# Kernel optimization log

Measured on AMD Instinct MI355X. Metric: run time of the kernel, lower is better.

Reference implementation:

```python
import jax, jax.numpy as jnp
import numpy as np

S, B, IN, H, NLAYERS = 2048, 1024, 4, 4, 6  # 3 stacked nn.LSTM modules x num_layers=2 each


def setup_inputs() -> dict:
    key = jax.random.key(0)
    ks = jax.random.split(key, 7)
    scale = 1.0 / np.sqrt(H)  # PyTorch LSTM init range
    return {
        "x": jax.random.normal(ks[0], (S, B, IN), jnp.float32),
        "w_ih": jax.random.uniform(ks[1], (NLAYERS, 4 * H, H), jnp.float32, -scale, scale),
        "w_hh": jax.random.uniform(ks[2], (NLAYERS, 4 * H, H), jnp.float32, -scale, scale),
        "b_ih": jax.random.uniform(ks[3], (NLAYERS, 4 * H), jnp.float32, -scale, scale),
        "b_hh": jax.random.uniform(ks[4], (NLAYERS, 4 * H), jnp.float32, -scale, scale),
        "reg_w": jax.random.uniform(ks[5], (1, H), jnp.float32, -scale, scale),
        "reg_b": jax.random.uniform(ks[6], (1,), jnp.float32, -scale, scale),
    }


def _lstm_layer(x, w_ih, w_hh, b_ih, b_hh):
    # x: [S, B, H_in]; PyTorch gate order: input, forget, cell(g), output
    b = x.shape[1]
    pre = jnp.einsum('sbi,gi->sbg', x, w_ih) + b_ih + b_hh  # [S, B, 4H], input projection hoisted out of scan

    def step(carry, p):
        h, c = carry
        gates = p + h @ w_hh.T
        i, f, g, o = jnp.split(gates, 4, axis=-1)
        c = jax.nn.sigmoid(f) * c + jax.nn.sigmoid(i) * jnp.tanh(g)
        h = jax.nn.sigmoid(o) * jnpat(c) if False else jax.nn.sigmoid(o) * jnp.tanh(c)
        return (h, c), h

    h0 = jnp.zeros((b, H), x.dtype)
    (_, _), ys = jax.lax.scan(step, (h0, h0), pre)
    return ys  # [S, B, H]


def reference(x, w_ih, w_hh, b_ih, b_hh, reg_w, reg_b):
    # 6 stacked LSTM layers (lstm1: layers 0-1, lstm2: 2-3, lstm3: 4-5).
    # Dropout (p=0.02) between layers and dropout3 are identity in eval mode.
    y = x
    for l in range(NLAYERS):
        y = _lstm_layer(y, w_ih[l], w_hh[l], b_ih[l], b_hh[l])
    out = jnp.einsum('sbh,oh->sbo', y, reg_w) + reg_b  # linear head, [S, B, 1]
    return out
```

## Files before the change

kernel.cpp:

```cpp
#include <hip/hip_runtime.h>

#define S_LEN  2048
#define BATCH  1024
#define NL     6
#define CH     16

typedef float f32x2 __attribute__((ext_vector_type(2)));

__device__ __forceinline__ float fexp2(float x) { return __builtin_amdgcn_exp2f(x); }
__device__ __forceinline__ float frcp(float x)  { return __builtin_amdgcn_rcpf(x); }

template <int CTRL>
__device__ __forceinline__ float dppf(float v) {
    return __int_as_float(__builtin_amdgcn_update_dpp(
        0, __float_as_int(v), CTRL, 0xF, 0xF, true));
}
__device__ __forceinline__ float bpermf(int addr, float v) {
    return __int_as_float(__builtin_amdgcn_ds_bpermute(addr, __float_as_int(v)));
}
__device__ __forceinline__ float swz4(float v) {
    return __int_as_float(__builtin_amdgcn_ds_swizzle(__float_as_int(v), 0x101F));
}
__device__ __forceinline__ f32x2 pkfma(f32x2 a, f32x2 b, f32x2 c) {
    f32x2 d;
    asm("v_pk_fma_f32 %0, %1, %2, %3" : "=v"(d) : "v"(a), "v"(b), "v"(c));
    return d;
}

__global__ __launch_bounds__(64, 1) void lstm_wavepipe(
    const float* __restrict__ x, const float* __restrict__ w_ih,
    const float* __restrict__ w_hh, const float* __restrict__ b_ih,
    const float* __restrict__ b_hh, const float* __restrict__ reg_w,
    const float* __restrict__ reg_b, float* __restrict__ out) {
    const int lane = threadIdx.x;
    const int L    = lane >> 3;
    const int q    = lane & 7;
    const int u    = q >> 1;
    const bool pOdd = (lane & 1);
    const int b    = blockIdx.x;
    const bool isFeeder = (L == 7);
    const bool isOut    = (lane == 48);

    const float KGc = -2.885390082f;
    const float KIc = -1.442695041f;

    f32x2 A1h[2], A2h[2], B1h[2], B2h[2], PB;
    if (L < NL) {
        const int gLoI = pOdd ? 2 : 0;
        const int gHiI = pOdd ? 3 : 1;
        const float klo = pOdd ? KGc : KIc;
        const float khi = KIc;
        const int rowLo = L * 16 + gLoI * 4 + u;
        const int rowHi = L * 16 + gHiI * 4 + u;
#pragma unroll
        for (int k = 0; k < 2; ++k) {
            const int c0 = u ^ (2 * k);
            const int c1 = u ^ (2 * k + 1);
            f32x2 a1, a2, b1, b2;
            a1.x = w_hh[rowLo * 4 + c0] * klo; a1.y = w_hh[rowHi * 4 + c1] * khi;
            a2.x = w_hh[rowHi * 4 + c0] * khi; a2.y = w_hh[rowLo * 4 + c1] * klo;
            b1.x = w_ih[rowLo * 4 + c0] * klo; b1.y = w_ih[rowHi * 4 + c1] * khi;
            b2.x = w_ih[rowHi * 4 + c0] * khi; b2.y = w_ih[rowLo * 4 + c1] * klo;
            A1h[k] = a1; A2h[k] = a2; B1h[k] = b1; B2h[k] = b2;
        }
        PB.x = (b_ih[rowLo] + b_hh[rowLo]) * klo;
        PB.y = (b_ih[rowHi] + b_hh[rowHi]) * khi;
    } else if (L == 6) {
#pragma unroll
        for (int k = 0; k < 2; ++k) {
            f32x2 z; z.x = 0.0f; z.y = 0.0f;
            A1h[k] = z; A2h[k] = z;
            f32x2 b1; b1.x = 0.0f; b1.y = reg_w[u ^ (2 * k + 1)];
            f32x2 b2; b2.x = reg_w[u ^ (2 * k)]; b2.y = 0.0f;
            B1h[k] = b1; B2h[k] = b2;
        }
        PB.x = 0.0f; PB.y = reg_b[0];
    } else {
#pragma unroll
        for (int k = 0; k < 2; ++k) {
            f32x2 z; z.x = 0.0f; z.y = 0.0f;
            A1h[k] = z; A2h[k] = z; B1h[k] = z; B2h[k] = z;
        }
        PB.x = 0.0f; PB.y = 0.0f;
    }
    const float aLo = pOdd ? 2.0f : KGc;
    const float bLo = pOdd ? -1.0f : 0.0f;
    f32x2 Z2; Z2.x = 0.0f; Z2.y = 0.0f;

    const int addrA = (((lane >= 8) ? (lane - 8) : (lane + 56)) << 2);

    float cp = 0.0f;
    f32x2 H;  H.x = 0.0f;  H.y = 0.0f;
    f32x2 H2; H2.x = 0.0f; H2.y = 0.0f;
    float bufP[CH], bufQ[CH], su[CH];
    const uint32_t xcol = (uint32_t)(b * 4 + u);
    uint32_t wi = xcol;
#pragma unroll
    for (int uu = 0; uu < CH; ++uu) { bufP[uu] = x[wi]; wi += 4096; }

    const float pub0 = isFeeder ? bufP[0] : 0.0f;
    const float pub1 = isFeeder ? bufP[1] : 0.0f;
    f32x2 E1c, E2c;
    {
        f32x2 U0, U20;
        U0.x = bpermf(addrA, pub0);
        U20.x = swz4(U0.x);
        U0.y  = dppf<0x4E>(U0.x);
        U20.y = dppf<0x4E>(U20.x);
        E1c = pkfma(B1h[1], U20, pkfma(B1h[0], U0, PB));
        E2c = pkfma(B2h[1], U20, pkfma(B2h[0], U0, Z2));
    }
    float hupN = bpermf(addrA, pub1);

#define STEP(u_, NXV_, MASKF_) do {                                            \
                                                     \
    H.y  = dppf<0x4E>(H.x);                                                    \
    H2.y = dppf<0x4E>(H2.x);                                                   \
                  \
    f32x2 F1 = pkfma(A1h[1], H2, E1c);                                         \
    f32x2 F2 = pkfma(A2h[1], H2, E2c);                                         \
    F1 = pkfma(A1h[0], H, F1);                                                 \
    F2 = pkfma(A2h[0], H, F2);                                                 \
    const float gLo = F1.x + F2.y;                                             \
    const float gHi = F1.y + F2.x;                                             \
              \
    f32x2 Un, U2n;                                                             \
    U2n.x = swz4(hupN);                                                        \
    Un.x  = hupN;                                                              \
    Un.y  = dppf<0x4E>(hupN);                                                  \
    f32x2 E1n = pkfma(B1h[0], Un, PB);                                         \
    f32x2 E2n = pkfma(B2h[0], Un, Z2);                                         \
    U2n.y = dppf<0x4E>(U2n.x);                                                 \
    E1n = pkfma(B1h[1], U2n, E1n);                                             \
    E2n = pkfma(B2h[1], U2n, E2n);                                             \
                                                              \
    const float rA = frcp(1.0f + fexp2(gLo));                                  \
    const float rB = frcp(1.0f + fexp2(gHi));                                  \
    const float sA = fmaf(aLo, rA, bLo);         \
    const float X  = dppf<0xB1>(sA);                                           \
    const float Y  = dppf<0xB1>(rB);                                           \
    const float fsel = pOdd ? Y : rB;            \
    const float ssel = pOdd ? rB : Y;            \
    const float prod = sA * X;                    \
    const float cnp  = fmaf(fsel, cp, prod);              \
    const float th   = fmaf(2.0f, frcp(1.0f + fexp2(cnp)), -1.0f);             \
    const float hn   = ssel * th;                                              \
    float hpost, cpost;                                                        \
    if (MASKF_) {                                                              \
        const bool act = (u_ >= 2 * L);         \
        cpost = act ? cnp : cp;                                                \
        hpost = act ? hn : H.x;                                                \
    } else { cpost = cnp; hpost = hn; }                                        \
    cp = cpost;                                                                \
    su[u_] = gHi;                                 \
                                                   \
    H2.x = swz4(hpost);                                 \
    const float hpub = isFeeder ? (NXV_) : hpost;                              \
    hupN = bpermf(addrA, hpub);                   \
    H.x = hpost;                                                               \
    E1c = E1n; E2c = E2n;                                                      \
} while (0)

#define RUN_CHUNK(cc_, cur_, nxt_, MASKF_, PREFM_, GUARDF_, NSTEPS_) do {      \
    if ((PREFM_) == 1) {                                                       \
        _Pragma("unroll")                                                      \
        for (int uu = 0; uu < CH; ++uu) { nxt_[uu] = x[wi]; wi += 4096; }      \
    } else if ((PREFM_) == 2) {                                                \
        const float xl = x[2047u * 4096u + xcol];                              \
        _Pragma("unroll")                                                      \
        for (int uu = 0; uu < CH; ++uu) nxt_[uu] = xl;                         \
    }                                                                          \
    _Pragma("unroll")                                                          \
    for (int uu = 0; uu < (NSTEPS_); ++uu) {                                   \
        if (uu < CH - 2)       STEP(uu, cur_[uu + 2], MASKF_);                 \
        else if (uu == CH - 2) STEP(uu, nxt_[0],      MASKF_);                 \
        else                   STEP(uu, nxt_[1],      MASKF_);                 \
    }                                                                          \
    if (isOut) {                                                               \
        const int base = (cc_) * CH - 12;     \
        _Pragma("unroll")                                                      \
        for (int uu = 0; uu < (NSTEPS_); ++uu) {                               \
            const int t = base + uu;                                           \
            if (!(GUARDF_) || ((t >= 0) && (t < S_LEN)))                       \
                out[(size_t)t * BATCH + b] = su[uu];                           \
        }                                                                      \
    }                                                                          \
} while (0)

    RUN_CHUNK(0, bufP, bufQ, 1, 1, 1, CH);
#pragma unroll 1
    for (int cc = 1; cc < 127; cc += 2) {
        RUN_CHUNK(cc,     bufQ, bufP, 0, 1, 0, CH);
        RUN_CHUNK(cc + 1, bufP, bufQ, 0, 1, 0, CH);
    }
    RUN_CHUNK(127, bufQ, bufP, 0, 2, 0, CH);
    RUN_CHUNK(128, bufP, bufQ, 0, 0, 0, 12);
#undef RUN_CHUNK
#undef STEP
}

extern "C" void kernel_launch(void* const* d_in, const int* in_sizes, int n_in,
                              void* d_out, int out_size, void* d_ws, size_t ws_size,
                              hipStream_t stream) {
    const float* x     = (const float*)d_in[0];
    const float* w_ih  = (const float*)d_in[1];
    const float* w_hh  = (const float*)d_in[2];
    const float* b_ih  = (const float*)d_in[3];
    const float* b_hh  = (const float*)d_in[4];
    const float* reg_w = (const float*)d_in[5];
    const float* reg_b = (const float*)d_in[6];
    float* out = (float*)d_out;

    dim3 grid(BATCH);
    dim3 block(64);
    hipLaunchKernelGGL(lstm_wavepipe, grid, block, 0, stream, x, w_ih, w_hh,
                       b_ih, b_hh, reg_w, reg_b, out);
}
```

Baseline: 324.7 us.

## Deepen cross-layer wavefront pipeline to three-step skew between stacked layers

Changes the layer-to-layer handoff so each layer consumes the previous layer's output from two steps earlier instead of one, which adds one extra pipeline stage per layer boundary. The input-projection terms for the next step no longer depend on a value broadcast in the same step, taking the bpermute latency off the recurrent critical path. It also folds the tanh rescale into a single fma with a pre-doubled output gate. In exchange the warm-up and drain grow (skew 3*L, output offset 18, two extra chunks) and more registers are live.

```diff
diff --git a/kernel.cpp b/kernel.cpp
--- a/kernel.cpp
+++ b/kernel.cpp
@@ -90,8 +90,7 @@
     const int addrA = (((lane >= 8) ? (lane - 8) : (lane + 56)) << 2);
 
     float cp = 0.0f;
-    f32x2 H;  H.x = 0.0f;  H.y = 0.0f;
-    f32x2 H2; H2.x = 0.0f; H2.y = 0.0f;
+    float Hx = 0.0f, H2x = 0.0f;
     float bufP[CH], bufQ[CH], su[CH];
     const uint32_t xcol = (uint32_t)(b * 4 + u);
     uint32_t wi = xcol;
@@ -100,39 +99,41 @@
 
     const float pub0 = isFeeder ? bufP[0] : 0.0f;
     const float pub1 = isFeeder ? bufP[1] : 0.0f;
+    const float pub2 = isFeeder ? bufP[2] : 0.0f;
     f32x2 E1c, E2c;
     {
-        f32x2 U0, U20;
-        U0.x = bpermf(addrA, pub0);
-        U20.x = swz4(U0.x);
-        U0.y  = dppf<0x4E>(U0.x);
-        U20.y = dppf<0x4E>(U20.x);
-        E1c = pkfma(B1h[1], U20, pkfma(B1h[0], U0, PB));
-        E2c = pkfma(B2h[1], U20, pkfma(B2h[0], U0, Z2));
+        const float h0 = bpermf(addrA, pub0);
+        f32x2 U0; U0.x = h0; U0.y = dppf<0x4E>(h0);
+        const float u20 = swz4(h0);
+        f32x2 U2; U2.x = u20; U2.y = dppf<0x4E>(u20);
+        E1c = pkfma(B1h[1], U2, pkfma(B1h[0], U0, PB));
+        E2c = pkfma(B2h[1], U2, pkfma(B2h[0], U0, Z2));
     }
-    float hupN = bpermf(addrA, pub1);
+    float hupE = bpermf(addrA, pub1);
+    float U2s  = swz4(hupE);
+    float hupM = bpermf(addrA, pub2);
 
 #define STEP(u_, NXV_, MASKF_) do {                                            \
-                                                     \
-    H.y  = dppf<0x4E>(H.x);                                                    \
-    H2.y = dppf<0x4E>(H2.x);                                                   \
-                  \
-    f32x2 F1 = pkfma(A1h[1], H2, E1c);                                         \
-    f32x2 F2 = pkfma(A2h[1], H2, E2c);                                         \
-    F1 = pkfma(A1h[0], H, F1);                                                 \
-    F2 = pkfma(A2h[0], H, F2);                                                 \
+      \
+    f32x2 Un, U2n;                                                             \
+    Un.x = hupE;  Un.y = dppf<0x4E>(hupE);                                     \
+    U2n.x = U2s;  U2n.y = dppf<0x4E>(U2s);                                     \
+    f32x2 E1n = pkfma(B1h[0], Un, PB);                                         \
+    f32x2 E2n = pkfma(B2h[0], Un, Z2);                                         \
+    E1n = pkfma(B1h[1], U2n, E1n);                                             \
+    E2n = pkfma(B2h[1], U2n, E2n);                                             \
+                      \
+    f32x2 Hh, H2h;                                                             \
+    Hh.x = Hx;   Hh.y = dppf<0x4E>(Hx);                                        \
+    H2h.x = H2x; H2h.y = dppf<0x4E>(H2x);                                      \
+    f32x2 F1 = pkfma(A1h[0], Hh, E1c);                                         \
+    f32x2 F2 = pkfma(A2h[0], Hh, E2c);                                         \
+    F1 = pkfma(A1h[1], H2h, F1);                                               \
+    F2 = pkfma(A2h[1], H2h, F2);                                               \
     const float gLo = F1.x + F2.y;                                             \
     const float gHi = F1.y + F2.x;                                             \
-              \
-    f32x2 Un, U2n;                                                             \
-    U2n.x = swz4(hupN);                                                        \
-    Un.x  = hupN;                                                              \
-    Un.y  = dppf<0x4E>(hupN);                                                  \
-    f32x2 E1n = pkfma(B1h[0], Un, PB);                                         \
-    f32x2 E2n = pkfma(B2h[0], Un, Z2);                                         \
-    U2n.y = dppf<0x4E>(U2n.x);                                                 \
-    E1n = pkfma(B1h[1], U2n, E1n);                                             \
-    E2n = pkfma(B2h[1], U2n, E2n);                                             \
+                 \
+    const float U2sN = swz4(hupM);                                             \
                                                               \
     const float rA = frcp(1.0f + fexp2(gLo));                                  \
     const float rB = frcp(1.0f + fexp2(gHi));                                  \
@@ -141,23 +142,24 @@
     const float Y  = dppf<0xB1>(rB);                                           \
     const float fsel = pOdd ? Y : rB;            \
     const float ssel = pOdd ? rB : Y;            \
+    const float ssel2 = ssel + ssel;            \
     const float prod = sA * X;                    \
     const float cnp  = fmaf(fsel, cp, prod);              \
-    const float th   = fmaf(2.0f, frcp(1.0f + fexp2(cnp)), -1.0f);             \
-    const float hn   = ssel * th;                                              \
+    const float rT   = frcp(1.0f + fexp2(cnp));                                \
+    const float hn   = fmaf(ssel2, rT, -ssel);            \
     float hpost, cpost;                                                        \
     if (MASKF_) {                                                              \
-        const bool act = (u_ >= 2 * L);         \
+        const bool act = (u_ >= 3 * L);         \
         cpost = act ? cnp : cp;                                                \
-        hpost = act ? hn : H.x;                                                \
+        hpost = act ? hn : Hx;                                                 \
     } else { cpost = cnp; hpost = hn; }                                        \
     cp = cpost;                                                                \
     su[u_] = gHi;                                 \
-                                                   \
-    H2.x = swz4(hpost);                                 \
+    const float H2xN = swz4(hpost);               \
     const float hpub = isFeeder ? (NXV_) : hpost;                              \
-    hupN = bpermf(addrA, hpub);                   \
-    H.x = hpost;                                                               \
+    const float hupNew = bpermf(addrA, hpub);                                  \
+    Hx = hpost; H2x = H2xN;                                                    \
+    hupE = hupM; hupM = hupNew; U2s = U2sN;                                    \
     E1c = E1n; E2c = E2n;                                                      \
 } while (0)
 
@@ -172,12 +174,11 @@
     }                                                                          \
     _Pragma("unroll")                                                          \
     for (int uu = 0; uu < (NSTEPS_); ++uu) {                                   \
-        if (uu < CH - 2)       STEP(uu, cur_[uu + 2], MASKF_);                 \
-        else if (uu == CH - 2) STEP(uu, nxt_[0],      MASKF_);                 \
-        else                   STEP(uu, nxt_[1],      MASKF_);                 \
+        if (uu < CH - 3) STEP(uu, cur_[uu + 3], MASKF_);                       \
+        else             STEP(uu, nxt_[uu + 3 - CH], MASKF_);                  \
     }                                                                          \
     if (isOut) {                                                               \
-        const int base = (cc_) * CH - 12;     \
+        const int base = (cc_) * CH - 18;     \
         _Pragma("unroll")                                                      \
         for (int uu = 0; uu < (NSTEPS_); ++uu) {                               \
             const int t = base + uu;                                           \
@@ -188,13 +189,16 @@
 } while (0)
 
     RUN_CHUNK(0, bufP, bufQ, 1, 1, 1, CH);
+    RUN_CHUNK(1, bufQ, bufP, 0, 1, 1, CH);
 #pragma unroll 1
-    for (int cc = 1; cc < 127; cc += 2) {
-        RUN_CHUNK(cc,     bufQ, bufP, 0, 1, 0, CH);
-        RUN_CHUNK(cc + 1, bufP, bufQ, 0, 1, 0, CH);
+    for (int cc = 2; cc < 126; cc += 2) {
+        RUN_CHUNK(cc,     bufP, bufQ, 0, 1, 0, CH);
+        RUN_CHUNK(cc + 1, bufQ, bufP, 0, 1, 0, CH);
     }
+    RUN_CHUNK(126, bufP, bufQ, 0, 1, 0, CH);
     RUN_CHUNK(127, bufQ, bufP, 0, 2, 0, CH);
-    RUN_CHUNK(128, bufP, bufQ, 0, 0, 0, 12);
+    RUN_CHUNK(128, bufP, bufQ, 0, 2, 0, CH);
+    RUN_CHUNK(129, bufQ, bufP, 0, 0, 0, 2);
 #undef RUN_CHUNK
 #undef STEP
 }
```

Result: no change. 325.4 us (+0.2%).
